# Kernel optimization log

Hardware: AMD Instinct MI355X
Metric: run time of the kernel (lower is better)

The kernel has to match this reference:

```python
import jax, jax.numpy as jnp
import numpy as np

B, S, D = 8, 1024, 1024
H, K = 16, 64  # num_heads, key_dim
NEG_INF = -1e9  # Keras _large_compatible_negative for float32


def setup_inputs() -> dict:
    key = jax.random.key(0)
    ks = jax.random.split(key, 10)
    x = jax.random.normal(ks[0], (B, S, D), dtype=jnp.float32)
    mask = jax.random.bernoulli(ks[1], 0.9, (B, S))  # bool per-token mask
    w = lambda k, shp: (0.02 * jax.random.normal(k, shp, dtype=jnp.float32))
    return {
        "input_tensor": x,
        "input_mask": mask,
        "Wq": w(ks[2], (D, H, K)), "bq": jnp.zeros((H, K), jnp.float32),
        "Wk": w(ks[3], (D, H, K)), "bk": jnp.zeros((H, K), jnp.float32),
        "Wv": w(ks[4], (D, H, K)), "bv": jnp.zeros((H, K), jnp.float32),
        "Wo": w(ks[5], (H, K, D)), "bo": jnp.zeros((D,), jnp.float32),
    }


def reference(input_tensor, input_mask, Wq, bq, Wk, bk, Wv, bv, Wo, bo):
    x = input_tensor
    # QKV projections: [B,S,D] x [D,H,K] -> [B,S,H,K]
    q = jnp.einsum("bsd,dhk->bshk", x, Wq) + bq
    k = jnp.einsum("bsd,dhk->bshk", x, Wk) + bk
    v = jnp.einsum("bsd,dhk->bshk", x, Wv) + bv
    # scaled dot-product scores: [B,H,Sq,Sk]
    scores = jnp.einsum("bqhk,bshk->bhqs", q, k) / jnp.sqrt(
        jnp.asarray(K, x.dtype))
    # mask = logical_and(mask[...,None], mask[...,None,:]) per example
    m2 = (input_mask[:, :, None] & input_mask[:, None, :])  # [B,Sq,Sk]
    scores = scores + (1.0 - m2[:, None, :, :].astype(x.dtype)) * NEG_INF
    probs = jax.nn.softmax(scores, axis=-1)
    # attend and project out: [B,S,H,K] -> [B,S,D]
    ctx = jnp.einsum("bhqs,bshk->bqhk", probs, v)
    return jnp.einsum("bqhk,hkd->bqd", ctx, Wo) + bo
```

## Files before the change

### kernel.cpp

```cpp
#include <hip/hip_runtime.h>
#include <math.h>

#define Ss 1024
#define Dd 1024
#define Hh 16
#define Kk 64

typedef __bf16 bf16x8 __attribute__((ext_vector_type(8)));
typedef __bf16 bf16x4 __attribute__((ext_vector_type(4)));
typedef float  f32x4  __attribute__((ext_vector_type(4)));

#define MFMA16(a, b, c) __builtin_amdgcn_mfma_f32_16x16x32_bf16(a, b, c, 0, 0, 0)

#define XB_E   8388608u
#define WT_E   3145728u
#define WOT_E  1048576u
#define QKV_E  8388608u

#define QSC 0.18033688011112042f

__device__ __forceinline__ float exp2_hw(float x) {
    float r; asm("v_exp_f32 %0, %1" : "=v"(r) : "v"(x)); return r;
}

typedef __attribute__((address_space(1))) const void gas_void;
typedef __attribute__((address_space(3))) void las_void;
__device__ __forceinline__ void gll16(const __bf16* g, char* l) {
    __builtin_amdgcn_global_load_lds((gas_void*)g, (las_void*)l, 16, 0, 0);
}

__global__ __launch_bounds__(256) void prep(
    const float* __restrict__ x,
    const float* __restrict__ Wq, const float* __restrict__ Wk,
    const float* __restrict__ Wv, const float* __restrict__ Wo,
    __bf16* __restrict__ xb, __bf16* __restrict__ WT, __bf16* __restrict__ WoT)
{
    __shared__ float tile[64][65];
    const int z = blockIdx.z;
    const int t = threadIdx.x;

    if (z == 4) {
        size_t blk = blockIdx.y * 16 + blockIdx.x;
        const float4* src = (const float4*)(x + blk * 32768);
        bf16x4* dst = (bf16x4*)(((__bf16*)xb) + blk * 32768);
        #pragma unroll
        for (int u = 0; u < 32; ++u) {
            float4 v = src[u * 256 + t];
            dst[u * 256 + t] =
                (bf16x4){(__bf16)v.x, (__bf16)v.y, (__bf16)v.z, (__bf16)v.w};
        }
        return;
    }

    const float* src = (z == 0) ? Wq : (z == 1) ? Wk : (z == 2) ? Wv : Wo;
    __bf16* dst = (z < 3) ? (WT + (size_t)z * 1048576) : WoT;

    int r0 = blockIdx.y * 64, c0 = blockIdx.x * 64;
    int rr = t >> 2, cg = (t & 3) * 16;

    #pragma unroll
    for (int u = 0; u < 4; ++u) {
        float4 v = *(const float4*)(src + (size_t)(r0 + rr) * 1024 + c0 + cg + u * 4);
        tile[rr][cg + u * 4 + 0] = v.x;
        tile[rr][cg + u * 4 + 1] = v.y;
        tile[rr][cg + u * 4 + 2] = v.z;
        tile[rr][cg + u * 4 + 3] = v.w;
    }
    __syncthreads();
    bf16x8 o0, o1;
    #pragma unroll
    for (int jj = 0; jj < 8; ++jj) o0[jj] = (__bf16)tile[cg + jj][rr];
    #pragma unroll
    for (int jj = 0; jj < 8; ++jj) o1[jj] = (__bf16)tile[cg + 8 + jj][rr];
    __bf16* dp = dst + (size_t)(c0 + rr) * 1024 + r0 + cg;
    *(bf16x8*)dp = o0;
    *(bf16x8*)(dp + 8) = o1;
}

template <int BN>
__global__ __launch_bounds__(512) void gemm_bt(
    const __bf16* __restrict__ A, const __bf16* __restrict__ Bt, int mode,
    __bf16* __restrict__ qb, __bf16* __restrict__ kb, __bf16* __restrict__ vb,
    const float* __restrict__ bq, const float* __restrict__ bk,
    const float* __restrict__ bv,
    float* __restrict__ outf, const float* __restrict__ bo)
{
    constexpr int NJ  = BN / 64;
    constexpr int NJH = NJ / 2;
    constexpr int WN  = BN / 4;

    __shared__ __align__(16) __bf16 As[2][256][64];
    __shared__ __align__(16) __bf16 Bs[2][BN][64];

    const int t = threadIdx.x;
    const int wave = t >> 6, lane = t & 63;
    const int quad = lane >> 4, l16 = lane & 15;
    const int wm = wave >> 2, wn = wave & 3;

    int g = blockIdx.y * gridDim.x + blockIdx.x;
    g = (g & 7) * 32 + (g >> 3);
    const int bx = g % gridDim.x, by = g / gridDim.x;
    const int m0 = by * 256, n0 = bx * BN;

    const int srow = t >> 3;
    const int scol = (((t & 7) ^ (srow & 7)) * 8);
    const __bf16* pa = A  + (size_t)(m0 + srow) * 1024 + scol;
    const __bf16* pb = Bt + (size_t)(n0 + srow) * 1024 + scol;
    char* lA = (char*)(&As[0][0][0]) + t * 16;
    char* lB = (char*)(&Bs[0][0][0]) + t * 16;

#define STAGE(slot, k0) do {                                                  \
        _Pragma("unroll")                                                     \
        for (int g_ = 0; g_ < 4; ++g_)                                        \
            gll16(pa + (k0) + g_ * 65536, lA + (slot) * 32768 + g_ * 8192);   \
        _Pragma("unroll")                                                     \
        for (int g_ = 0; g_ < BN / 64; ++g_)                                  \
            gll16(pb + (k0) + g_ * 65536, lB + (slot) * (BN * 128) + g_ * 8192); \
    } while (0)

    STAGE(0, 0);

    f32x4 acc[8][NJ];
    #pragma unroll
    for (int i = 0; i < 8; ++i)
        #pragma unroll
        for (int j = 0; j < NJ; ++j) acc[i][j] = (f32x4){0.f, 0.f, 0.f, 0.f};

    const int swz = (l16 & 7) << 4;

    for (int it = 0; it < 16; ++it) {
        const int s = it & 1;
        asm volatile("s_waitcnt vmcnt(0)" ::: "memory");
        __builtin_amdgcn_s_barrier();
        if (it < 15) STAGE(s ^ 1, (it + 1) * 64);

        const char* baseA = (const char*)&As[s][0][0];
        const char* baseB = (const char*)&Bs[s][0][0];

        #pragma unroll
        for (int mh = 0; mh < 2; ++mh) {
            bf16x8 afr[4][2];
            #pragma unroll
            for (int mi = 0; mi < 4; ++mi) {
                int rowa = (wm * 128 + (mh * 4 + mi) * 16 + l16) * 128;
                afr[mi][0] = *(const bf16x8*)(baseA + rowa + ((quad * 16) ^ swz));
                afr[mi][1] = *(const bf16x8*)(baseA + rowa + ((64 + quad * 16) ^ swz));
            }
            #pragma unroll
            for (int nh = 0; nh < 2; ++nh) {
                bf16x8 bfr[NJH][2];
                #pragma unroll
                for (int nj = 0; nj < NJH; ++nj) {
                    int rowb = (wn * WN + (nh * NJH + nj) * 16 + l16) * 128;
                    bfr[nj][0] = *(const bf16x8*)(baseB + rowb + ((quad * 16) ^ swz));
                    bfr[nj][1] = *(const bf16x8*)(baseB + rowb + ((64 + quad * 16) ^ swz));
                }
                __builtin_amdgcn_s_setprio(1);
                #pragma unroll
                for (int mi = 0; mi < 4; ++mi)
                    #pragma unroll
                    for (int nj = 0; nj < NJH; ++nj)
                        acc[mh * 4 + mi][nh * NJH + nj] =
                            MFMA16(afr[mi][1], bfr[nj][1],
                            MFMA16(afr[mi][0], bfr[nj][0],
                                   acc[mh * 4 + mi][nh * NJH + nj]));
                __builtin_amdgcn_s_setprio(0);
            }
            if (mh == 0) __builtin_amdgcn_s_barrier();
        }
    }
#undef STAGE

    if (mode == 0) {
        #pragma unroll
        for (int mi = 0; mi < 8; ++mi) {
            int row = m0 + wm * 128 + mi * 16 + quad * 4;
            int b = row >> 10, sx = row & 1023;
            #pragma unroll
            for (int nj = 0; nj < NJ; ++nj) {
                int c16 = n0 + wn * WN + nj * 16;
                int z = c16 >> 10;
                int n1 = (c16 + l16) & 1023;
                int h = n1 >> 6, ch = n1 & 63;
                if (z == 0) {
                    float bia = bq[n1];
                    __bf16* dst = qb + ((size_t)(b * Hh + h) * Ss + sx) * Kk + ch;
                    #pragma unroll
                    for (int r = 0; r < 4; ++r)
                        dst[(size_t)r * Kk] = (__bf16)((acc[mi][nj][r] + bia) * QSC);
                } else if (z == 1) {
                    float bia = bk[n1];
                    __bf16* dst = kb + ((size_t)(b * Hh + h) * Ss + sx) * Kk + ch;
                    #pragma unroll
                    for (int r = 0; r < 4; ++r)
                        dst[(size_t)r * Kk] = (__bf16)(acc[mi][nj][r] + bia);
                } else {
                    float bia = bv[n1];
                    bf16x4 o;
                    #pragma unroll
                    for (int r = 0; r < 4; ++r) o[r] = (__bf16)(acc[mi][nj][r] + bia);
                    *(bf16x4*)(vb + ((size_t)(b * Hh + h) * Kk + ch) * Ss + sx) = o;
                }
            }
        }
    } else {
        #pragma unroll
        for (int mi = 0; mi < 8; ++mi) {
            int row = m0 + wm * 128 + mi * 16 + quad * 4;
            #pragma unroll
            for (int nj = 0; nj < NJ; ++nj) {
                int n = n0 + wn * WN + nj * 16 + l16;
                float bia = bo[n];
                #pragma unroll
                for (int r = 0; r < 4; ++r)
                    outf[(size_t)(row + r) * 1024 + n] = acc[mi][nj][r] + bia;
            }
        }
    }
}

__global__ __launch_bounds__(256) void attn(
    const __bf16* __restrict__ qb, const __bf16* __restrict__ kb,
    const __bf16* __restrict__ vb, const int* __restrict__ mask,
    __bf16* __restrict__ ctx)
{
    const int bh = blockIdx.x;
    const int q0 = blockIdx.y * 128;
    const int b  = bh >> 4;
    const int h  = bh & 15;
    const size_t base = (size_t)bh * Ss * Kk;

    __shared__ __align__(16) __bf16 Qs[128][72];
    __shared__ __align__(16) __bf16 Ks[2][64][72];
    __shared__ __align__(16) __bf16 VTs[2][64][72];
    __shared__ __align__(16) __bf16 Ps[4][32][72];
    __shared__ float mkf[1024];

    const int t    = threadIdx.x;
    const int wave = t >> 6, lane = t & 63;
    const int quad = lane >> 4, l16 = lane & 15;
    const int qbase = wave * 32;

    #pragma unroll
    for (int p = 0; p < 4; ++p) {
        int idx = t + p * 256;
        int r = idx >> 3, g = idx & 7;
        *(bf16x8*)&Qs[r][g * 8] =
            *(const bf16x8*)(qb + base + (size_t)(q0 + r) * Kk + g * 8);
    }
    {
        int4 mi = *(const int4*)(mask + b * Ss + t * 4);
        mkf[t * 4 + 0] = (float)mi.x;
        mkf[t * 4 + 1] = (float)mi.y;
        mkf[t * 4 + 2] = (float)mi.z;
        mkf[t * 4 + 3] = (float)mi.w;
    }

    const int r0 = t >> 3, c0 = (t & 7) * 8;
    bf16x8 kr0, kr1, vr0, vr1;
    kr0 = *(const bf16x8*)(kb + base + (size_t)(r0) * Kk + c0);
    kr1 = *(const bf16x8*)(kb + base + (size_t)(r0 + 32) * Kk + c0);
    vr0 = *(const bf16x8*)(vb + base + (size_t)(r0) * Ss + c0);
    vr1 = *(const bf16x8*)(vb + base + (size_t)(r0 + 32) * Ss + c0);

    __syncthreads();

    bf16x8 aq[2][2];
    #pragma unroll
    for (int rg = 0; rg < 2; ++rg) {
        aq[rg][0] = *(const bf16x8*)&Qs[qbase + rg * 16 + l16][quad * 8];
        aq[rg][1] = *(const bf16x8*)&Qs[qbase + rg * 16 + l16][32 + quad * 8];
    }
    float mqf[2][4], omqf[2][4];
    #pragma unroll
    for (int rg = 0; rg < 2; ++rg)
        #pragma unroll
        for (int i = 0; i < 4; ++i) {
            float m = mkf[q0 + qbase + rg * 16 + quad * 4 + i];
            mqf[rg][i] = m; omqf[rg][i] = 1.0f - m;
        }

    f32x4 O[2][4];
    float lsum[2][4];
    #pragma unroll
    for (int rg = 0; rg < 2; ++rg)
        #pragma unroll
        for (int nb = 0; nb < 4; ++nb) O[rg][nb] = (f32x4){0.f, 0.f, 0.f, 0.f};
    #pragma unroll
    for (int rg = 0; rg < 2; ++rg)
        #pragma unroll
        for (int i = 0; i < 4; ++i) lsum[rg][i] = 0.f;

    for (int kt = 0; kt < Ss; kt += 64) {
        const int p = (kt >> 6) & 1;
        *(bf16x8*)&Ks[p][r0][c0] = kr0;
        *(bf16x8*)&Ks[p][r0 + 32][c0] = kr1;
        *(bf16x8*)&VTs[p][r0][c0] = vr0;
        *(bf16x8*)&VTs[p][r0 + 32][c0] = vr1;
        __syncthreads();

        int ktn = kt + 64;
        if (ktn < Ss) {
            kr0 = *(const bf16x8*)(kb + base + (size_t)(ktn + r0) * Kk + c0);
            kr1 = *(const bf16x8*)(kb + base + (size_t)(ktn + r0 + 32) * Kk + c0);
            vr0 = *(const bf16x8*)(vb + base + (size_t)(r0) * Ss + ktn + c0);
            vr1 = *(const bf16x8*)(vb + base + (size_t)(r0 + 32) * Ss + ktn + c0);
        }

        float mkv[4];
        #pragma unroll
        for (int nb = 0; nb < 4; ++nb) mkv[nb] = mkf[kt + nb * 16 + l16];

        bf16x8 kb0[4], kb1[4];
        #pragma unroll
        for (int nb = 0; nb < 4; ++nb) {
            kb0[nb] = *(const bf16x8*)&Ks[p][nb * 16 + l16][quad * 8];
            kb1[nb] = *(const bf16x8*)&Ks[p][nb * 16 + l16][32 + quad * 8];
        }

        f32x4 s[2][4];
        __builtin_amdgcn_s_setprio(1);
        #pragma unroll
        for (int rg = 0; rg < 2; ++rg)
            #pragma unroll
            for (int nb = 0; nb < 4; ++nb) {
                f32x4 a = (f32x4){0.f, 0.f, 0.f, 0.f};
                a = MFMA16(aq[rg][0], kb0[nb], a);
                a = MFMA16(aq[rg][1], kb1[nb], a);
                s[rg][nb] = a;
            }
        __builtin_amdgcn_s_setprio(0);

        #pragma unroll
        for (int rg = 0; rg < 2; ++rg)
            #pragma unroll
            for (int i = 0; i < 4; ++i) {
                float ls = 0.f;
                #pragma unroll
                for (int nb = 0; nb < 4; ++nb) {
                    float pv = exp2_hw(s[rg][nb][i]) * mkv[nb];
                    pv = pv * mqf[rg][i] + omqf[rg][i];
                    Ps[wave][rg * 16 + quad * 4 + i][nb * 16 + l16] = (__bf16)pv;
                    ls += pv;
                }
                lsum[rg][i] += ls;
            }

        bf16x8 ap0[2], ap1[2];
        #pragma unroll
        for (int rg = 0; rg < 2; ++rg) {
            ap0[rg] = *(const bf16x8*)&Ps[wave][rg * 16 + l16][quad * 8];
            ap1[rg] = *(const bf16x8*)&Ps[wave][rg * 16 + l16][32 + quad * 8];
        }
        __builtin_amdgcn_s_setprio(1);
        #pragma unroll
        for (int nb = 0; nb < 4; ++nb) {
            bf16x8 vb0 = *(const bf16x8*)&VTs[p][nb * 16 + l16][quad * 8];
            bf16x8 vb1 = *(const bf16x8*)&VTs[p][nb * 16 + l16][32 + quad * 8];
            #pragma unroll
            for (int rg = 0; rg < 2; ++rg) {
                O[rg][nb] = MFMA16(ap0[rg], vb0, O[rg][nb]);
                O[rg][nb] = MFMA16(ap1[rg], vb1, O[rg][nb]);
            }
        }
        __builtin_amdgcn_s_setprio(0);
    }

    #pragma unroll
    for (int rg = 0; rg < 2; ++rg)
        #pragma unroll
        for (int i = 0; i < 4; ++i) {
            float l = lsum[rg][i];
            l += __shfl_xor(l, 1);
            l += __shfl_xor(l, 2);
            l += __shfl_xor(l, 4);
            l += __shfl_xor(l, 8);
            float inv = 1.0f / l;
            int srow = q0 + qbase + rg * 16 + quad * 4 + i;
            __bf16* dst = ctx + ((size_t)(b * Ss + srow) * Hh + h) * Kk;
            #pragma unroll
            for (int nb = 0; nb < 4; ++nb)
                dst[nb * 16 + l16] = (__bf16)(O[rg][nb][i] * inv);
        }
}

extern "C" void kernel_launch(void* const* d_in, const int* in_sizes, int n_in,
                              void* d_out, int out_size, void* d_ws, size_t ws_size,
                              hipStream_t stream) {
    const float* x    = (const float*)d_in[0];
    const int*   mask = (const int*)d_in[1];
    const float* Wq   = (const float*)d_in[2];
    const float* bq   = (const float*)d_in[3];
    const float* Wk   = (const float*)d_in[4];
    const float* bk   = (const float*)d_in[5];
    const float* Wv   = (const float*)d_in[6];
    const float* bv   = (const float*)d_in[7];
    const float* Wo   = (const float*)d_in[8];
    const float* bo   = (const float*)d_in[9];

    __bf16* xb   = (__bf16*)d_ws;
    __bf16* WT   = xb + XB_E;
    __bf16* WoT  = WT + WT_E;
    __bf16* qb   = WoT + WOT_E;
    __bf16* kb   = qb + QKV_E;
    __bf16* vb   = kb + QKV_E;
    __bf16* ctxb = vb + QKV_E;
    float* out = (float*)d_out;

    prep<<<dim3(16, 16, 5), 256, 0, stream>>>(x, Wq, Wk, Wv, Wo, xb, WT, WoT);
    gemm_bt<384><<<dim3(8, 32), 512, 0, stream>>>(xb, WT, 0, qb, kb, vb,
                                                  bq, bk, bv, nullptr, nullptr);
    attn<<<dim3(128, 8), 256, 0, stream>>>(qb, kb, vb, mask, ctxb);
    gemm_bt<128><<<dim3(8, 32), 512, 0, stream>>>(ctxb, WoT, 1, nullptr, nullptr,
                                                  nullptr, nullptr, nullptr,
                                                  nullptr, out, bo);
}
```

Measured before the change: 266.6 us.

## Restructure GEMM main loop into quadrant-staged pipeline with finer prefetch interleaving

Rewrites the bf16 GEMM main loop to split each K-step into quadrant phases. Global-to-LDS loads for the next stage are issued in pieces between the phases and waited on with partial vmcnt counts, so prefetch overlaps MFMA work instead of draining fully each iteration. The QKV projection moves from BN=384 on an 8x32 grid to BN=256 on a 12x32 grid, and the block-swizzle stride now derives from the grid size. This adds more barriers and fragile hand-tuned wait counts, and changes the wave count and register use per tile.

```diff
diff --git a/kernel.cpp b/kernel.cpp
--- a/kernel.cpp
+++ b/kernel.cpp
@@ -85,9 +85,9 @@
     const float* __restrict__ bv,
     float* __restrict__ outf, const float* __restrict__ bo)
 {
-    constexpr int NJ  = BN / 64;
-    constexpr int NJH = NJ / 2;
-    constexpr int WN  = BN / 4;
+    constexpr int NB = BN / 64;
+    constexpr int NJ = BN / 64;
+    constexpr int WN = BN / 4;
 
     __shared__ __align__(16) __bf16 As[2][256][64];
     __shared__ __align__(16) __bf16 Bs[2][BN][64];
@@ -97,8 +97,10 @@
     const int quad = lane >> 4, l16 = lane & 15;
     const int wm = wave >> 2, wn = wave & 3;
 
+    const int nwg = gridDim.x * gridDim.y;
+    const int cpx = nwg >> 3;
     int g = blockIdx.y * gridDim.x + blockIdx.x;
-    g = (g & 7) * 32 + (g >> 3);
+    g = (g & 7) * cpx + (g >> 3);
     const int bx = g % gridDim.x, by = g / gridDim.x;
     const int m0 = by * 256, n0 = bx * BN;
 
@@ -109,16 +111,13 @@
     char* lA = (char*)(&As[0][0][0]) + t * 16;
     char* lB = (char*)(&Bs[0][0][0]) + t * 16;
 
-#define STAGE(slot, k0) do {                                                  \
-        _Pragma("unroll")                                                     \
-        for (int g_ = 0; g_ < 4; ++g_)                                        \
-            gll16(pa + (k0) + g_ * 65536, lA + (slot) * 32768 + g_ * 8192);   \
-        _Pragma("unroll")                                                     \
-        for (int g_ = 0; g_ < BN / 64; ++g_)                                  \
-            gll16(pb + (k0) + g_ * 65536, lB + (slot) * (BN * 128) + g_ * 8192); \
-    } while (0)
-
-    STAGE(0, 0);
+#define SGA(slot, k0, c) gll16(pa + (k0) + (c) * 65536, lA + (slot) * 32768 + (c) * 8192)
+#define SGB(slot, k0, c) gll16(pb + (k0) + (c) * 65536, lB + (slot) * (BN * 128) + (c) * 8192)
+
+    SGA(0, 0, 0); SGA(0, 0, 2);
+    #pragma unroll
+    for (int c = 0; c < NB; ++c) SGB(0, 0, c);
+    SGA(0, 0, 1); SGA(0, 0, 3);
 
     f32x4 acc[8][NJ];
     #pragma unroll
@@ -128,48 +127,150 @@
 
     const int swz = (l16 & 7) << 4;
 
+    asm volatile("s_waitcnt vmcnt(2)" ::: "memory");
+    __syncthreads();
+
     for (int it = 0; it < 16; ++it) {
-        const int s = it & 1;
-        asm volatile("s_waitcnt vmcnt(0)" ::: "memory");
-        __builtin_amdgcn_s_barrier();
-        if (it < 15) STAGE(s ^ 1, (it + 1) * 64);
-
+        const int s = it & 1, ns = s ^ 1;
+        const int kn = (it + 1) * 64;
+        const bool st = (it < 15);
         const char* baseA = (const char*)&As[s][0][0];
         const char* baseB = (const char*)&Bs[s][0][0];
 
-        #pragma unroll
-        for (int mh = 0; mh < 2; ++mh) {
-            bf16x8 afr[4][2];
+        bf16x8 af[4][2], b0f[2][2], b1f[2][2];
+
+        if constexpr (BN == 256) {
             #pragma unroll
             for (int mi = 0; mi < 4; ++mi) {
-                int rowa = (wm * 128 + (mh * 4 + mi) * 16 + l16) * 128;
-                afr[mi][0] = *(const bf16x8*)(baseA + rowa + ((quad * 16) ^ swz));
-                afr[mi][1] = *(const bf16x8*)(baseA + rowa + ((64 + quad * 16) ^ swz));
-            }
-            #pragma unroll
-            for (int nh = 0; nh < 2; ++nh) {
-                bf16x8 bfr[NJH][2];
-                #pragma unroll
-                for (int nj = 0; nj < NJH; ++nj) {
-                    int rowb = (wn * WN + (nh * NJH + nj) * 16 + l16) * 128;
-                    bfr[nj][0] = *(const bf16x8*)(baseB + rowb + ((quad * 16) ^ swz));
-                    bfr[nj][1] = *(const bf16x8*)(baseB + rowb + ((64 + quad * 16) ^ swz));
-                }
-                __builtin_amdgcn_s_setprio(1);
-                #pragma unroll
-                for (int mi = 0; mi < 4; ++mi)
-                    #pragma unroll
-                    for (int nj = 0; nj < NJH; ++nj)
-                        acc[mh * 4 + mi][nh * NJH + nj] =
-                            MFMA16(afr[mi][1], bfr[nj][1],
-                            MFMA16(afr[mi][0], bfr[nj][0],
-                                   acc[mh * 4 + mi][nh * NJH + nj]));
-                __builtin_amdgcn_s_setprio(0);
-            }
-            if (mh == 0) __builtin_amdgcn_s_barrier();
-        }
-    }
-#undef STAGE
+                int ra = (wm * 128 + mi * 16 + l16) * 128;
+                af[mi][0] = *(const bf16x8*)(baseA + ra + ((quad * 16) ^ swz));
+                af[mi][1] = *(const bf16x8*)(baseA + ra + ((64 + quad * 16) ^ swz));
+            }
+            #pragma unroll
+            for (int nj = 0; nj < 2; ++nj) {
+                int rb = (wn * 64 + nj * 16 + l16) * 128;
+                b0f[nj][0] = *(const bf16x8*)(baseB + rb + ((quad * 16) ^ swz));
+                b0f[nj][1] = *(const bf16x8*)(baseB + rb + ((64 + quad * 16) ^ swz));
+            }
+            if (st) { SGA(ns, kn, 0); SGA(ns, kn, 2); SGB(ns, kn, 0); SGB(ns, kn, 1); }
+            __builtin_amdgcn_s_barrier();
+            asm volatile("s_waitcnt lgkmcnt(0)" ::: "memory");
+            __builtin_amdgcn_sched_barrier(0);
+            __builtin_amdgcn_s_setprio(1);
+            #pragma unroll
+            for (int mi = 0; mi < 4; ++mi)
+                #pragma unroll
+                for (int nj = 0; nj < 2; ++nj)
+                    acc[mi][nj] = MFMA16(af[mi][1], b0f[nj][1],
+                                  MFMA16(af[mi][0], b0f[nj][0], acc[mi][nj]));
+            __builtin_amdgcn_s_setprio(0);
+            __builtin_amdgcn_s_barrier();
+
+            if (it == 15) asm volatile("s_waitcnt vmcnt(0)" ::: "memory");
+            else          asm volatile("s_waitcnt vmcnt(4)" ::: "memory");
+            #pragma unroll
+            for (int nj = 0; nj < 2; ++nj) {
+                int rb = (wn * 64 + (2 + nj) * 16 + l16) * 128;
+                b1f[nj][0] = *(const bf16x8*)(baseB + rb + ((quad * 16) ^ swz));
+                b1f[nj][1] = *(const bf16x8*)(baseB + rb + ((64 + quad * 16) ^ swz));
+            }
+            if (st) { SGB(ns, kn, 2); SGB(ns, kn, 3); }
+            __builtin_amdgcn_s_barrier();
+            asm volatile("s_waitcnt lgkmcnt(0)" ::: "memory");
+            __builtin_amdgcn_sched_barrier(0);
+            __builtin_amdgcn_s_setprio(1);
+            #pragma unroll
+            for (int mi = 0; mi < 4; ++mi)
+                #pragma unroll
+                for (int nj = 0; nj < 2; ++nj)
+                    acc[mi][2 + nj] = MFMA16(af[mi][1], b1f[nj][1],
+                                      MFMA16(af[mi][0], b1f[nj][0], acc[mi][2 + nj]));
+            __builtin_amdgcn_s_setprio(0);
+            __builtin_amdgcn_s_barrier();
+
+            #pragma unroll
+            for (int mi = 0; mi < 4; ++mi) {
+                int ra = (wm * 128 + (4 + mi) * 16 + l16) * 128;
+                af[mi][0] = *(const bf16x8*)(baseA + ra + ((quad * 16) ^ swz));
+                af[mi][1] = *(const bf16x8*)(baseA + ra + ((64 + quad * 16) ^ swz));
+            }
+            if (st) { SGA(ns, kn, 1); SGA(ns, kn, 3); }
+            __builtin_amdgcn_s_barrier();
+            asm volatile("s_waitcnt lgkmcnt(0)" ::: "memory");
+            __builtin_amdgcn_sched_barrier(0);
+            __builtin_amdgcn_s_setprio(1);
+            #pragma unroll
+            for (int mi = 0; mi < 4; ++mi)
+                #pragma unroll
+                for (int nj = 0; nj < 2; ++nj)
+                    acc[4 + mi][nj] = MFMA16(af[mi][1], b0f[nj][1],
+                                      MFMA16(af[mi][0], b0f[nj][0], acc[4 + mi][nj]));
+            __builtin_amdgcn_s_setprio(0);
+            __builtin_amdgcn_s_barrier();
+
+            asm volatile("s_waitcnt vmcnt(2)" ::: "memory");
+            __builtin_amdgcn_s_barrier();
+            __builtin_amdgcn_s_setprio(1);
+            #pragma unroll
+            for (int mi = 0; mi < 4; ++mi)
+                #pragma unroll
+                for (int nj = 0; nj < 2; ++nj)
+                    acc[4 + mi][2 + nj] = MFMA16(af[mi][1], b1f[nj][1],
+                                          MFMA16(af[mi][0], b1f[nj][0], acc[4 + mi][2 + nj]));
+            __builtin_amdgcn_s_setprio(0);
+            __builtin_amdgcn_s_barrier();
+        } else {
+            asm volatile("s_waitcnt vmcnt(0)" ::: "memory");
+            #pragma unroll
+            for (int mi = 0; mi < 4; ++mi) {
+                int ra = (wm * 128 + mi * 16 + l16) * 128;
+                af[mi][0] = *(const bf16x8*)(baseA + ra + ((quad * 16) ^ swz));
+                af[mi][1] = *(const bf16x8*)(baseA + ra + ((64 + quad * 16) ^ swz));
+            }
+            #pragma unroll
+            for (int nj = 0; nj < 2; ++nj) {
+                int rb = (wn * 32 + nj * 16 + l16) * 128;
+                b0f[nj][0] = *(const bf16x8*)(baseB + rb + ((quad * 16) ^ swz));
+                b0f[nj][1] = *(const bf16x8*)(baseB + rb + ((64 + quad * 16) ^ swz));
+            }
+            if (st) { SGA(ns, kn, 0); SGA(ns, kn, 2); SGB(ns, kn, 0); SGB(ns, kn, 1); }
+            __builtin_amdgcn_s_barrier();
+            asm volatile("s_waitcnt lgkmcnt(0)" ::: "memory");
+            __builtin_amdgcn_sched_barrier(0);
+            __builtin_amdgcn_s_setprio(1);
+            #pragma unroll
+            for (int mi = 0; mi < 4; ++mi)
+                #pragma unroll
+                for (int nj = 0; nj < 2; ++nj)
+                    acc[mi][nj] = MFMA16(af[mi][1], b0f[nj][1],
+                                  MFMA16(af[mi][0], b0f[nj][0], acc[mi][nj]));
+            __builtin_amdgcn_s_setprio(0);
+            __builtin_amdgcn_s_barrier();
+
+            asm volatile("s_waitcnt vmcnt(0)" ::: "memory");
+            #pragma unroll
+            for (int mi = 0; mi < 4; ++mi) {
+                int ra = (wm * 128 + (4 + mi) * 16 + l16) * 128;
+                af[mi][0] = *(const bf16x8*)(baseA + ra + ((quad * 16) ^ swz));
+                af[mi][1] = *(const bf16x8*)(baseA + ra + ((64 + quad * 16) ^ swz));
+            }
+            if (st) { SGA(ns, kn, 1); SGA(ns, kn, 3); }
+            __builtin_amdgcn_s_barrier();
+            asm volatile("s_waitcnt lgkmcnt(0)" ::: "memory");
+            __builtin_amdgcn_sched_barrier(0);
+            __builtin_amdgcn_s_setprio(1);
+            #pragma unroll
+            for (int mi = 0; mi < 4; ++mi)
+                #pragma unroll
+                for (int nj = 0; nj < 2; ++nj)
+                    acc[4 + mi][nj] = MFMA16(af[mi][1], b0f[nj][1],
+                                      MFMA16(af[mi][0], b0f[nj][0], acc[4 + mi][nj]));
+            __builtin_amdgcn_s_setprio(0);
+            __builtin_amdgcn_s_barrier();
+        }
+    }
+#undef SGA
+#undef SGB
 
     if (mode == 0) {
         #pragma unroll
@@ -408,8 +509,8 @@
     float* out = (float*)d_out;
 
     prep<<<dim3(16, 16, 5), 256, 0, stream>>>(x, Wq, Wk, Wv, Wo, xb, WT, WoT);
-    gemm_bt<384><<<dim3(8, 32), 512, 0, stream>>>(xb, WT, 0, qb, kb, vb,
-                                                  bq, bk, bv, nullptr, nullptr);
+    gemm_bt<256><<<dim3(12, 32), 512, 0, stream>>>(xb, WT, 0, qb, kb, vb,
+                                                   bq, bk, bv, nullptr, nullptr);
     attn<<<dim3(128, 8), 256, 0, stream>>>(qb, kb, vb, mask, ctxb);
     gemm_bt<128><<<dim3(8, 32), 512, 0, stream>>>(ctxb, WoT, 1, nullptr, nullptr,
                                                   nullptr, nullptr, nullptr,
```

Measured after the change: 263.0 us. No clear change (-1.3%).
